# Optimization experiments

Measured on AMD Instinct MI355X. Metric: run time of the kernel, lower is better.

Reference implementation:

```python
import jax, jax.numpy as jnp
import numpy as np

B, N, D_NODE, D_EDGE, D_GRAPH = 2, 1024, 128, 16, 128
MID, OUT = 64, 128


def _linear_params(key, fan_in, fan_out):
    # haiku Linear default: truncated-normal(stddev=1/sqrt(fan_in)) weight, zero bias
    w = jax.random.normal(key, (fan_in, fan_out), dtype=jnp.float32) / np.sqrt(fan_in)
    b = jnp.zeros((fan_out,), dtype=jnp.float32)
    return w, b


def setup_inputs() -> dict:
    key = jax.random.key(0)
    ks = jax.random.split(key, 12)
    features = jax.random.normal(ks[0], (B, N, D_NODE), dtype=jnp.float32)
    e_features = jax.random.normal(ks[1], (B, N, N, D_EDGE), dtype=jnp.float32)
    g_features = jax.random.normal(ks[2], (B, D_GRAPH), dtype=jnp.float32)
    adj = jax.random.randint(ks[3], (B, N, N), 0, 2).astype(jnp.float32)
    # ensure self-loops so every row has at least one valid neighbor
    adj = jnp.maximum(adj, jnp.eye(N, dtype=jnp.float32)[None])
    Wm, bm = _linear_params(ks[4], D_NODE, OUT)
    Wskip, bskip = _linear_params(ks[5], D_NODE, OUT)
    W1, b1 = _linear_params(ks[6], D_NODE, MID)
    W2, b2 = _linear_params(ks[7], D_NODE, MID)
    We, be = _linear_params(ks[8], D_EDGE, MID)
    Wg, bg = _linear_params(ks[9], D_GRAPH, MID)
    Wa, ba = _linear_params(ks[10], MID, 1)
    return dict(features=features, e_features=e_features, g_features=g_features,
                adj=adj, Wm=Wm, bm=bm, Wskip=Wskip, bskip=bskip,
                W1=W1, b1=b1, W2=W2, b2=b2, We=We, be=be, Wg=Wg, bg=bg,
                Wa=Wa, ba=ba)


def reference(features, e_features, g_features, adj,
              Wm, bm, Wskip, bskip, W1, b1, W2, b2, We, be, Wg, bg, Wa, ba):
    # bias mask: 0 where edge exists, -1e9 where not
    bias_mat = (adj - 1.0) * 1e9  # (b,n,n)

    values = features @ Wm + bm          # (b,n,out)
    pre_att_1 = features @ W1 + b1       # (b,n,mid) -> per-target j
    pre_att_2 = features @ W2 + b2       # (b,n,mid) -> per-source i
    pre_att_e = e_features @ We + be     # (b,n,n,mid)
    pre_att_g = g_features @ Wg + bg     # (b,mid)

    # pre_att[b,i,j] = p1[b,j] + p2[b,i] + pe[b,i,j] + pg[b]
    pre_att = (pre_att_1[:, None, :, :] + pre_att_2[:, :, None, :]
               + pre_att_e + pre_att_g[:, None, None, :])  # (b,n,n,mid)

    logits = jnp.squeeze(jax.nn.leaky_relu(pre_att) @ Wa + ba, axis=-1)  # (b,n,n)
    coefs = jax.nn.softmax(logits + bias_mat, axis=-1)                   # (b,n,n)

    ret = jnp.matmul(coefs, values)       # (b,n,out)
    ret = ret + (features @ Wskip + bskip)  # residual
    return jax.nn.relu(ret)               # activation=relu
```

## Files before the change

kernel.cpp:

```cpp
#include <hip/hip_runtime.h>
#include <hip/hip_bf16.h>
#include <cstdint>

#define B_   2
#define N_   1024
#define DN_  128
#define DE_  16
#define DG_  128
#define MID_ 64
#define OUT_ 128
#define TI_  4
#define PR_ROWS 4

typedef short bf16x8 __attribute__((ext_vector_type(8)));
typedef float f32x4  __attribute__((ext_vector_type(4)));

__device__ inline short f2bf(float f) {
    union { float f; unsigned u; } v; v.f = f;
    unsigned r = v.u + 0x7FFFu + ((v.u >> 16) & 1u);
    return (short)(unsigned short)(r >> 16);
}

__device__ inline unsigned pk2(float lo, float hi) {
    union { __hip_bfloat162 h; unsigned u; } p;
    p.h = __float22bfloat162_rn(make_float2(lo, hi));
    return p.u;
}

__global__ void __launch_bounds__(384) prep_all(
    const float* __restrict__ features, const float* __restrict__ g_features,
    const float* __restrict__ Wm, const float* __restrict__ bm,
    const float* __restrict__ Wskip, const float* __restrict__ bskip,
    const float* __restrict__ W1, const float* __restrict__ b1,
    const float* __restrict__ W2, const float* __restrict__ b2,
    const float* __restrict__ We, const float* __restrict__ be,
    const float* __restrict__ Wg, const float* __restrict__ bg,
    float* __restrict__ values, float* __restrict__ skipo,
    float* __restrict__ P1x, float* __restrict__ p2,
    float* __restrict__ pg, short* __restrict__ We_frag)
{
    const int t   = threadIdx.x;
    const int blk = blockIdx.x;

    if (blk == 512) {
        for (int e = t; e < 4 * 64 * 8; e += 384) {
            const int c    = e >> 9;
            const int lane = (e >> 3) & 63;
            const int j    = e & 7;
            const int quad = lane >> 4, s = lane & 15;
            short v = 0;
            if (quad < 2) v = f2bf(We[(quad * 8 + j) * MID_ + c * 16 + s]);
            We_frag[e] = v;
        }
        return;
    }
    if (blk == 513) {
        if (t < MID_) {
            float a0 = bg[t], a1 = bg[t];
            for (int k = 0; k < DG_; ++k) {
                const float w = Wg[k * MID_ + t];
                a0 += g_features[k] * w;
                a1 += g_features[DG_ + k] * w;
            }
            pg[t] = a0; pg[MID_ + t] = a1;
        }
        return;
    }

    const int r0 = blk * PR_ROWS;
    __shared__ float feat[PR_ROWS][DN_];
    for (int idx = t; idx < PR_ROWS * DN_; idx += 384)
        feat[idx >> 7][idx & 127] = features[(size_t)r0 * DN_ + idx];
    __syncthreads();

    const float* W; int c, stride; float base; float* outp; int ostride;
    if (t < 128) {
        W = Wm;    c = t;       stride = OUT_; base = bm[c];
        outp = values + (size_t)r0 * OUT_ + c; ostride = OUT_;
    } else if (t < 256) {
        W = Wskip; c = t - 128; stride = OUT_; base = bskip[c];
        outp = skipo + (size_t)r0 * OUT_ + c;  ostride = OUT_;
    } else if (t < 320) {
        W = W1;    c = t - 256; stride = MID_; base = b1[c] + be[c];
        outp = P1x + (size_t)r0 * MID_ + c;    ostride = MID_;
    } else {
        W = W2;    c = t - 320; stride = MID_; base = b2[c];
        outp = p2 + (size_t)r0 * MID_ + c;     ostride = MID_;
    }

    float acc[PR_ROWS] = {};
    for (int k = 0; k < DN_; ++k) {
        const float w = W[k * stride + c];
        #pragma unroll
        for (int q = 0; q < PR_ROWS; ++q) acc[q] += feat[q][k] * w;
    }
    #pragma unroll
    for (int q = 0; q < PR_ROWS; ++q) outp[q * ostride] = acc[q] + base;
}

__global__ void __launch_bounds__(512, 4) gat_main(
    const float* __restrict__ e_features, const float* __restrict__ adj,
    const short* __restrict__ We_frag, const float* __restrict__ Wa,
    const float* __restrict__ ba,
    const float* __restrict__ values, const float* __restrict__ skipo,
    const float* __restrict__ P1x, const float* __restrict__ p2,
    const float* __restrict__ pg, float* __restrict__ out)
{
    const int t    = threadIdx.x;
    const int wv   = t >> 6;
    const int l    = t & 63;
    const int quad = l >> 4;
    const int s    = l & 15;
    const int r    = blockIdx.x;
    const int b    = r >> 8;
    const int i0   = (r & 255) * TI_;

    __shared__ float lgT[N_][8];
    __shared__ float redv[8][16][33];
    __shared__ float sinv[TI_];

    bf16x8 bfr[4];
    float  wa_r[4], p2i[TI_][4];
    #pragma unroll
    for (int c = 0; c < 4; ++c) {
        bfr[c]  = *(const bf16x8*)&We_frag[(c * 64 + l) * 8];
        wa_r[c] = Wa[c * 16 + s];
        const float pgc = pg[b * MID_ + c * 16 + s];
        #pragma unroll
        for (int ii = 0; ii < TI_; ++ii)
            p2i[ii][c] = p2[((size_t)(b * N_ + i0 + ii)) * MID_ + c * 16 + s] + pgc;
    }
    const float ba0 = ba[0];

    for (int tile = wv; tile < N_ / 16; tile += 8) {
        const int j0 = tile * 16;
        float base[4][4];
        {
            const float* pb = &P1x[((size_t)(b * N_ + j0 + quad * 4)) * MID_ + s];
            #pragma unroll
            for (int c = 0; c < 4; ++c)
                #pragma unroll
                for (int rr = 0; rr < 4; ++rr)
                    base[c][rr] = pb[rr * MID_ + c * 16];
        }
        for (int ii = 0; ii < TI_; ++ii) {
            const size_t rb = ((size_t)(b * N_ + i0 + ii)) * (size_t)N_;
            union { bf16x8 v; unsigned u[4]; } a;
            a.u[0] = a.u[1] = a.u[2] = a.u[3] = 0u;
            if (quad < 2) {
                const float* ep = &e_features[(rb + j0 + s) * DE_ + quad * 8];
                const float4 u0 = *(const float4*)ep;
                const float4 u1 = *(const float4*)(ep + 4);
                a.u[0] = pk2(u0.x, u0.y);
                a.u[1] = pk2(u0.z, u0.w);
                a.u[2] = pk2(u1.x, u1.y);
                a.u[3] = pk2(u1.z, u1.w);
            }
            f32x4 acc[4];
            #pragma unroll
            for (int c = 0; c < 4; ++c)
                #pragma unroll
                for (int rr = 0; rr < 4; ++rr)
                    acc[c][rr] = base[c][rr] + p2i[ii][c];
            #pragma unroll
            for (int c = 0; c < 4; ++c)
                acc[c] = __builtin_amdgcn_mfma_f32_16x16x32_bf16(a.v, bfr[c], acc[c], 0, 0, 0);

            float tt[4];
            #pragma unroll
            for (int rr = 0; rr < 4; ++rr) {
                float x0 = acc[0][rr]; x0 = fmaxf(x0, 0.01f * x0);
                float x1 = acc[1][rr]; x1 = fmaxf(x1, 0.01f * x1);
                float x2 = acc[2][rr]; x2 = fmaxf(x2, 0.01f * x2);
                float x3 = acc[3][rr]; x3 = fmaxf(x3, 0.01f * x3);
                tt[rr] = x0 * wa_r[0] + x1 * wa_r[1] + x2 * wa_r[2] + x3 * wa_r[3];
            }
            #pragma unroll
            for (int o = 1; o < 16; o <<= 1) {
                tt[0] += __shfl_xor(tt[0], o);
                tt[1] += __shfl_xor(tt[1], o);
                tt[2] += __shfl_xor(tt[2], o);
                tt[3] += __shfl_xor(tt[3], o);
            }
            if (s < 4) {
                const int j = j0 + quad * 4 + s;
                const float av = adj[rb + j];
                lgT[j][ii] = tt[s] + ba0 + (av - 1.0f) * 1e9f;
            }
        }
    }
    __syncthreads();

    if (wv < TI_) {
        float v[16];
        float m = -3.4e38f;
        #pragma unroll
        for (int q = 0; q < 16; ++q) {
            v[q] = lgT[l + 64 * q][wv];
            m = fmaxf(m, v[q]);
        }
        #pragma unroll
        for (int o = 1; o < 64; o <<= 1) m = fmaxf(m, __shfl_xor(m, o));
        float sum = 0.f;
        #pragma unroll
        for (int q = 0; q < 16; ++q) {
            const float e = __expf(v[q] - m);
            lgT[l + 64 * q][wv] = e;
            sum += e;
        }
        #pragma unroll
        for (int o = 1; o < 64; o <<= 1) sum += __shfl_xor(sum, o);
        if (l == 0) sinv[wv] = 1.0f / sum;
    }
    __syncthreads();

    const int cg  = t & 15;
    const int jp  = t >> 4;
    const int ch0 = cg * 8;
    float acc[TI_][8] = {};
    const float* vbase = values + (size_t)b * N_ * OUT_ + ch0;
    for (int j = jp; j < N_; j += 32) {
        const float4 cf = *(const float4*)&lgT[j][0];
        const float* vp = vbase + (size_t)j * OUT_;
        const float4 v0 = *(const float4*)vp;
        const float4 v1 = *(const float4*)(vp + 4);
        const float vv[8] = {v0.x, v0.y, v0.z, v0.w, v1.x, v1.y, v1.z, v1.w};
        const float cw[4] = {cf.x, cf.y, cf.z, cf.w};
        #pragma unroll
        for (int ii = 0; ii < TI_; ++ii)
            #pragma unroll
            for (int k = 0; k < 8; ++k)
                acc[ii][k] += cw[ii] * vv[k];
    }
    #pragma unroll
    for (int ii = 0; ii < TI_; ++ii)
        #pragma unroll
        for (int k = 0; k < 8; ++k) {
            acc[ii][k] += __shfl_xor(acc[ii][k], 16);
            acc[ii][k] += __shfl_xor(acc[ii][k], 32);
        }
    if (l < 16) {
        #pragma unroll
        for (int ii = 0; ii < TI_; ++ii)
            #pragma unroll
            for (int k = 0; k < 8; ++k)
                redv[wv][l][ii * 8 + k] = acc[ii][k];
    }
    __syncthreads();
    {
        const int ii = t >> 7;
        const int ch = t & 127;
        const int g  = ch >> 3, k = ch & 7;
        float sum = 0.f;
        #pragma unroll
        for (int w = 0; w < 8; ++w) sum += redv[w][g][ii * 8 + k];
        const size_t ob = ((size_t)(b * N_ + i0 + ii)) * OUT_ + ch;
        out[ob] = fmaxf(sum * sinv[ii] + skipo[ob], 0.f);
    }
}

extern "C" void kernel_launch(void* const* d_in, const int* in_sizes, int n_in,
                              void* d_out, int out_size, void* d_ws, size_t ws_size,
                              hipStream_t stream) {
    const float* features   = (const float*)d_in[0];
    const float* e_features = (const float*)d_in[1];
    const float* g_features = (const float*)d_in[2];
    const float* adj        = (const float*)d_in[3];
    const float* Wm    = (const float*)d_in[4];
    const float* bm    = (const float*)d_in[5];
    const float* Wskip = (const float*)d_in[6];
    const float* bskip = (const float*)d_in[7];
    const float* W1    = (const float*)d_in[8];
    const float* b1    = (const float*)d_in[9];
    const float* W2    = (const float*)d_in[10];
    const float* b2    = (const float*)d_in[11];
    const float* We    = (const float*)d_in[12];
    const float* be    = (const float*)d_in[13];
    const float* Wg    = (const float*)d_in[14];
    const float* bg    = (const float*)d_in[15];
    const float* Wa    = (const float*)d_in[16];
    const float* ba    = (const float*)d_in[17];
    float* out = (float*)d_out;

    float* ws      = (float*)d_ws;
    float* values  = ws;
    float* skipo   = ws + 262144;
    float* P1x     = ws + 524288;
    float* p2      = ws + 655360;
    float* pg      = ws + 786432;
    short* We_frag = (short*)(ws + 786560);

    prep_all<<<B_ * N_ / PR_ROWS + 2, 384, 0, stream>>>(
        features, g_features, Wm, bm, Wskip, bskip, W1, b1, W2, b2,
        We, be, Wg, bg, values, skipo, P1x, p2, pg, We_frag);
    gat_main<<<B_ * N_ / TI_, 512, 0, stream>>>(
        e_features, adj, We_frag, Wa, ba, values, skipo, P1x, p2, pg, out);
}
```

Measured before the change: 329.3 us.

## Restructure GAT main kernel with register-prefetched edges, 256 threads, masked softmax

Shrinks the block to 256 threads and restructures the edge-logit loop so each wave prefetches the next tile's edge features for all four rows into registers while computing the current tile, hiding global latency. The adjacency mask moves from the per-tile store into a vectorised softmax pass that reads adj as float4 and zeros masked entries. The bias ba is dropped since softmax is shift-invariant. Block-to-row mapping interleaves batches, and the logit buffer is transposed to row-major with a narrower reduction. This raises register pressure from the prefetch buffers and gives fewer waves per block to hide latency.

```diff
diff --git a/kernel.cpp b/kernel.cpp
--- a/kernel.cpp
+++ b/kernel.cpp
@@ -98,10 +98,9 @@
     for (int q = 0; q < PR_ROWS; ++q) outp[q * ostride] = acc[q] + base;
 }
 
-__global__ void __launch_bounds__(512, 4) gat_main(
+__global__ void __launch_bounds__(256) gat_main(
     const float* __restrict__ e_features, const float* __restrict__ adj,
     const short* __restrict__ We_frag, const float* __restrict__ Wa,
-    const float* __restrict__ ba,
     const float* __restrict__ values, const float* __restrict__ skipo,
     const float* __restrict__ P1x, const float* __restrict__ p2,
     const float* __restrict__ pg, float* __restrict__ out)
@@ -112,11 +111,11 @@
     const int quad = l >> 4;
     const int s    = l & 15;
     const int r    = blockIdx.x;
-    const int b    = r >> 8;
-    const int i0   = (r & 255) * TI_;
-
-    __shared__ float lgT[N_][8];
-    __shared__ float redv[8][16][33];
+    const int b    = (r >> 2) & 1;
+    const int i0   = (((r >> 3) << 2) | (r & 3)) * TI_;
+
+    __shared__ float lgP[TI_][N_];
+    __shared__ float redv[TI_][16][36];
     __shared__ float sinv[TI_];
 
     bf16x8 bfr[4];
@@ -130,49 +129,75 @@
         for (int ii = 0; ii < TI_; ++ii)
             p2i[ii][c] = p2[((size_t)(b * N_ + i0 + ii)) * MID_ + c * 16 + s] + pgc;
     }
-    const float ba0 = ba[0];
-
-    for (int tile = wv; tile < N_ / 16; tile += 8) {
-        const int j0 = tile * 16;
+    const size_t erow0 = (size_t)(b * N_ + i0) * N_;
+
+    float4 eA[TI_][2];
+    if (quad < 2) {
+        #pragma unroll
+        for (int ii = 0; ii < TI_; ++ii) {
+            const float* ep = &e_features[(erow0 + (size_t)ii * N_ + wv * 16 + s) * DE_ + quad * 8];
+            eA[ii][0] = *(const float4*)ep;
+            eA[ii][1] = *(const float4*)(ep + 4);
+        }
+    }
+    for (int it = 0; it < 16; ++it) {
+        const int tile = wv + it * 4;
+        const int j0   = tile * 16;
+
+        unsigned af[TI_][4];
+        #pragma unroll
+        for (int ii = 0; ii < TI_; ++ii) {
+            if (quad < 2) {
+                af[ii][0] = pk2(eA[ii][0].x, eA[ii][0].y);
+                af[ii][1] = pk2(eA[ii][0].z, eA[ii][0].w);
+                af[ii][2] = pk2(eA[ii][1].x, eA[ii][1].y);
+                af[ii][3] = pk2(eA[ii][1].z, eA[ii][1].w);
+            } else {
+                af[ii][0] = af[ii][1] = af[ii][2] = af[ii][3] = 0u;
+            }
+        }
+        if (it < 15) {
+            const int jn = (tile + 4) * 16;
+            if (quad < 2) {
+                #pragma unroll
+                for (int ii = 0; ii < TI_; ++ii) {
+                    const float* ep = &e_features[(erow0 + (size_t)ii * N_ + jn + s) * DE_ + quad * 8];
+                    eA[ii][0] = *(const float4*)ep;
+                    eA[ii][1] = *(const float4*)(ep + 4);
+                }
+            }
+        }
         float base[4][4];
         {
-            const float* pb = &P1x[((size_t)(b * N_ + j0 + quad * 4)) * MID_ + s];
+            const float* pb = &P1x[((size_t)(b * N_) + j0 + quad * 4) * MID_ + s];
             #pragma unroll
             for (int c = 0; c < 4; ++c)
                 #pragma unroll
                 for (int rr = 0; rr < 4; ++rr)
                     base[c][rr] = pb[rr * MID_ + c * 16];
         }
+        #pragma unroll
         for (int ii = 0; ii < TI_; ++ii) {
-            const size_t rb = ((size_t)(b * N_ + i0 + ii)) * (size_t)N_;
-            union { bf16x8 v; unsigned u[4]; } a;
-            a.u[0] = a.u[1] = a.u[2] = a.u[3] = 0u;
-            if (quad < 2) {
-                const float* ep = &e_features[(rb + j0 + s) * DE_ + quad * 8];
-                const float4 u0 = *(const float4*)ep;
-                const float4 u1 = *(const float4*)(ep + 4);
-                a.u[0] = pk2(u0.x, u0.y);
-                a.u[1] = pk2(u0.z, u0.w);
-                a.u[2] = pk2(u1.x, u1.y);
-                a.u[3] = pk2(u1.z, u1.w);
-            }
+            union { unsigned u[4]; bf16x8 v; } a;
+            a.u[0] = af[ii][0]; a.u[1] = af[ii][1];
+            a.u[2] = af[ii][2]; a.u[3] = af[ii][3];
             f32x4 acc[4];
             #pragma unroll
-            for (int c = 0; c < 4; ++c)
-                #pragma unroll
-                for (int rr = 0; rr < 4; ++rr)
-                    acc[c][rr] = base[c][rr] + p2i[ii][c];
-            #pragma unroll
-            for (int c = 0; c < 4; ++c)
+            for (int c = 0; c < 4; ++c) {
+                acc[c] = (f32x4){0.f, 0.f, 0.f, 0.f};
                 acc[c] = __builtin_amdgcn_mfma_f32_16x16x32_bf16(a.v, bfr[c], acc[c], 0, 0, 0);
-
+            }
             float tt[4];
             #pragma unroll
             for (int rr = 0; rr < 4; ++rr) {
-                float x0 = acc[0][rr]; x0 = fmaxf(x0, 0.01f * x0);
-                float x1 = acc[1][rr]; x1 = fmaxf(x1, 0.01f * x1);
-                float x2 = acc[2][rr]; x2 = fmaxf(x2, 0.01f * x2);
-                float x3 = acc[3][rr]; x3 = fmaxf(x3, 0.01f * x3);
+                float x0 = acc[0][rr] + base[0][rr] + p2i[ii][0];
+                float x1 = acc[1][rr] + base[1][rr] + p2i[ii][1];
+                float x2 = acc[2][rr] + base[2][rr] + p2i[ii][2];
+                float x3 = acc[3][rr] + base[3][rr] + p2i[ii][3];
+                x0 = fmaxf(x0, 0.01f * x0);
+                x1 = fmaxf(x1, 0.01f * x1);
+                x2 = fmaxf(x2, 0.01f * x2);
+                x3 = fmaxf(x3, 0.01f * x3);
                 tt[rr] = x0 * wa_r[0] + x1 * wa_r[1] + x2 * wa_r[2] + x3 * wa_r[3];
             }
             #pragma unroll
@@ -182,31 +207,40 @@
                 tt[2] += __shfl_xor(tt[2], o);
                 tt[3] += __shfl_xor(tt[3], o);
             }
-            if (s < 4) {
-                const int j = j0 + quad * 4 + s;
-                const float av = adj[rb + j];
-                lgT[j][ii] = tt[s] + ba0 + (av - 1.0f) * 1e9f;
-            }
+            if (s < 4) lgP[ii][j0 + quad * 4 + s] = tt[s];
         }
     }
     __syncthreads();
 
-    if (wv < TI_) {
-        float v[16];
-        float m = -3.4e38f;
-        #pragma unroll
-        for (int q = 0; q < 16; ++q) {
-            v[q] = lgT[l + 64 * q][wv];
-            m = fmaxf(m, v[q]);
+    {
+        const size_t arb = (size_t)(b * N_ + i0 + wv) * N_;
+        float4 lv[4], av[4];
+        #pragma unroll
+        for (int q = 0; q < 4; ++q) {
+            lv[q] = *(const float4*)&lgP[wv][l * 4 + 256 * q];
+            av[q] = *(const float4*)&adj[arb + l * 4 + 256 * q];
+        }
+        const float NEG = -3.4e38f;
+        float m = NEG;
+        #pragma unroll
+        for (int q = 0; q < 4; ++q) {
+            m = fmaxf(m, av[q].x > 0.f ? lv[q].x : NEG);
+            m = fmaxf(m, av[q].y > 0.f ? lv[q].y : NEG);
+            m = fmaxf(m, av[q].z > 0.f ? lv[q].z : NEG);
+            m = fmaxf(m, av[q].w > 0.f ? lv[q].w : NEG);
         }
         #pragma unroll
         for (int o = 1; o < 64; o <<= 1) m = fmaxf(m, __shfl_xor(m, o));
         float sum = 0.f;
         #pragma unroll
-        for (int q = 0; q < 16; ++q) {
-            const float e = __expf(v[q] - m);
-            lgT[l + 64 * q][wv] = e;
-            sum += e;
+        for (int q = 0; q < 4; ++q) {
+            float4 e4;
+            e4.x = av[q].x > 0.f ? __expf(lv[q].x - m) : 0.f;
+            e4.y = av[q].y > 0.f ? __expf(lv[q].y - m) : 0.f;
+            e4.z = av[q].z > 0.f ? __expf(lv[q].z - m) : 0.f;
+            e4.w = av[q].w > 0.f ? __expf(lv[q].w - m) : 0.f;
+            *(float4*)&lgP[wv][l * 4 + 256 * q] = e4;
+            sum += (e4.x + e4.y) + (e4.z + e4.w);
         }
         #pragma unroll
         for (int o = 1; o < 64; o <<= 1) sum += __shfl_xor(sum, o);
@@ -214,48 +248,53 @@
     }
     __syncthreads();
 
-    const int cg  = t & 15;
-    const int jp  = t >> 4;
-    const int ch0 = cg * 8;
+    const int cg = l & 15, jp = l >> 4, ch0 = cg * 8;
     float acc[TI_][8] = {};
-    const float* vbase = values + (size_t)b * N_ * OUT_ + ch0;
-    for (int j = jp; j < N_; j += 32) {
-        const float4 cf = *(const float4*)&lgT[j][0];
-        const float* vp = vbase + (size_t)j * OUT_;
+    const float* vb = values + (size_t)b * N_ * OUT_ + ch0;
+    for (int k = 0; k < 64; ++k) {
+        const int j = wv * 4 + jp + k * 16;
+        float cw[TI_];
+        #pragma unroll
+        for (int ii = 0; ii < TI_; ++ii) cw[ii] = lgP[ii][j];
+        const float* vp = vb + (size_t)j * OUT_;
         const float4 v0 = *(const float4*)vp;
         const float4 v1 = *(const float4*)(vp + 4);
         const float vv[8] = {v0.x, v0.y, v0.z, v0.w, v1.x, v1.y, v1.z, v1.w};
-        const float cw[4] = {cf.x, cf.y, cf.z, cf.w};
         #pragma unroll
         for (int ii = 0; ii < TI_; ++ii)
             #pragma unroll
-            for (int k = 0; k < 8; ++k)
-                acc[ii][k] += cw[ii] * vv[k];
+            for (int kk = 0; kk < 8; ++kk)
+                acc[ii][kk] += cw[ii] * vv[kk];
     }
     #pragma unroll
     for (int ii = 0; ii < TI_; ++ii)
         #pragma unroll
-        for (int k = 0; k < 8; ++k) {
-            acc[ii][k] += __shfl_xor(acc[ii][k], 16);
-            acc[ii][k] += __shfl_xor(acc[ii][k], 32);
+        for (int kk = 0; kk < 8; ++kk) {
+            acc[ii][kk] += __shfl_xor(acc[ii][kk], 16);
+            acc[ii][kk] += __shfl_xor(acc[ii][kk], 32);
         }
     if (l < 16) {
         #pragma unroll
         for (int ii = 0; ii < TI_; ++ii)
             #pragma unroll
-            for (int k = 0; k < 8; ++k)
-                redv[wv][l][ii * 8 + k] = acc[ii][k];
+            for (int q = 0; q < 2; ++q) {
+                float4 w4 = make_float4(acc[ii][q * 4], acc[ii][q * 4 + 1],
+                                        acc[ii][q * 4 + 2], acc[ii][q * 4 + 3]);
+                *(float4*)&redv[wv][l][ii * 8 + q * 4] = w4;
+            }
     }
     __syncthreads();
     {
-        const int ii = t >> 7;
-        const int ch = t & 127;
-        const int g  = ch >> 3, k = ch & 7;
-        float sum = 0.f;
-        #pragma unroll
-        for (int w = 0; w < 8; ++w) sum += redv[w][g][ii * 8 + k];
-        const size_t ob = ((size_t)(b * N_ + i0 + ii)) * OUT_ + ch;
-        out[ob] = fmaxf(sum * sinv[ii] + skipo[ob], 0.f);
+        const int ch = t & 127, g = ch >> 3, kk = ch & 7;
+        const int iib = t >> 7;
+        #pragma unroll
+        for (int p = 0; p < 2; ++p) {
+            const int ii = iib + p * 2;
+            const float sum = redv[0][g][ii * 8 + kk] + redv[1][g][ii * 8 + kk]
+                            + redv[2][g][ii * 8 + kk] + redv[3][g][ii * 8 + kk];
+            const size_t ob = ((size_t)(b * N_ + i0 + ii)) * OUT_ + ch;
+            out[ob] = fmaxf(sum * sinv[ii] + skipo[ob], 0.f);
+        }
     }
 }
 
@@ -279,7 +318,6 @@
     const float* Wg    = (const float*)d_in[14];
     const float* bg    = (const float*)d_in[15];
     const float* Wa    = (const float*)d_in[16];
-    const float* ba    = (const float*)d_in[17];
     float* out = (float*)d_out;
 
     float* ws      = (float*)d_ws;
@@ -293,6 +331,6 @@
     prep_all<<<B_ * N_ / PR_ROWS + 2, 384, 0, stream>>>(
         features, g_features, Wm, bm, Wskip, bskip, W1, b1, W2, b2,
         We, be, Wg, bg, values, skipo, P1x, p2, pg, We_frag);
-    gat_main<<<B_ * N_ / TI_, 512, 0, stream>>>(
-        e_features, adj, We_frag, Wa, ba, values, skipo, P1x, p2, pg, out);
-}
+    gat_main<<<B_ * N_ / TI_, 256, 0, stream>>>(
+        e_features, adj, We_frag, Wa, values, skipo, P1x, p2, pg, out);
+}
```

Measured after the change: 297.9 us. 1.11x faster.
